# Optimization experiments

Measured on AMD Instinct MI355X. Metric: run time of the kernel, lower is better.

Reference implementation:

```python
import jax, jax.numpy as jnp
import numpy as np
from jax import lax
from jax.scipy.special import logsumexp

XY, Z, V, WS = 16, 8, 10000, 2
S = XY * XY * Z            # 2048 states
EMB, TOK, HID = 256, 100, 256
B, T, L = 8, 16, 12
EPS = 1e-5


def residual(x, w1, b1, w2, b2, g, beta):
    # ResidualLayer: relu(lin1) -> relu(lin2) -> LayerNorm(x2 + x1)
    x1 = jax.nn.relu(x @ w1.T + b1)
    x2 = jax.nn.relu(x1 @ w2.T + b2)
    h = x2 + x1
    mu = h.mean(-1, keepdims=True)
    var = ((h - mu) ** 2).mean(-1, keepdims=True)
    return (h - mu) * lax.rsqrt(var + EPS) * g + beta


def win_logmean(m, axis, ws):
    win = 2 * ws + 1
    pads = [(0, 0)] * m.ndim
    pads[axis] = (ws, ws)
    p = jnp.pad(m, pads, mode='edge')
    d = m.shape[axis]
    acc = lax.dynamic_slice_in_dim(p, 0, d, axis)
    for k in range(1, win):
        acc = jnp.logaddexp(acc, lax.dynamic_slice_in_dim(p, k, d, axis))
    return acc - jnp.log(jnp.float32(win))


def setup_inputs() -> dict:
    key = jax.random.key(0)
    it = iter(jax.random.split(key, 64))

    def rn(shape, scale=0.05):
        return jax.random.normal(next(it), shape, jnp.float32) * scale

    inp = {}
    inp['state_emb'] = jax.random.normal(next(it), (S, EMB), jnp.float32)
    inp['tok_emb'] = jax.random.normal(next(it), (V, TOK), jnp.float32)

    def res(pfx, din, dout):
        inp[pfx + '_w1'] = rn((dout, din))
        inp[pfx + '_b1'] = jnp.zeros((dout,), jnp.float32)
        inp[pfx + '_w2'] = rn((dout, dout))
        inp[pfx + '_b2'] = jnp.zeros((dout,), jnp.float32)
        inp[pfx + '_g'] = jnp.ones((dout,), jnp.float32)
        inp[pfx + '_beta'] = jnp.zeros((dout,), jnp.float32)

    res('start', EMB, HID)
    inp['start_wo'] = rn((1, HID))
    inp['start_bo'] = jnp.zeros((1,), jnp.float32)
    res('tin', EMB, HID)
    res('tout', EMB, HID)
    res('emit', EMB, TOK)
    inp['stories'] = jax.random.randint(next(it), (B, T, L), 0, V + 1)  # id V = pad
    inp['story_length'] = T
    return inp


def reference(state_emb, tok_emb,
              start_w1, start_b1, start_w2, start_b2, start_g, start_beta, start_wo, start_bo,
              tin_w1, tin_b1, tin_w2, tin_b2, tin_g, tin_beta,
              tout_w1, tout_b1, tout_w2, tout_b2, tout_g, tout_beta,
              emit_w1, emit_b1, emit_w2, emit_b2, emit_g, emit_beta,
              stories, story_length):
    # prior_log_p: [S]
    h0 = residual(state_emb, start_w1, start_b1, start_w2, start_b2, start_g, start_beta)
    priors = jax.nn.log_softmax((h0 @ start_wo.T + start_bo)[:, 0], axis=-1)

    # transition_log_p: sparse-neighbor masked [S,S] log-softmax
    h_in = residual(state_emb, tin_w1, tin_b1, tin_w2, tin_b2, tin_g, tin_beta)
    h_out = residual(state_emb, tout_w1, tout_b1, tout_w2, tout_b2, tout_g, tout_beta)
    trans = h_in @ h_out.T
    idx = jnp.arange(S)
    offs = jnp.array([0, 1, -1, XY, -XY, XY * XY, 2 * XY * XY])
    neigh = idx[:, None] + offs[None, :]                        # [S,7]
    allowed = (neigh[:, :, None] == idx[None, None, :]).any(1)  # allowed[j,i]
    trans = jax.nn.log_softmax(jnp.where(allowed, trans, -jnp.inf), axis=-1)

    # emission matrix with windowed log-mean pooling over x,y
    h_emit = residual(state_emb, emit_w1, emit_b1, emit_w2, emit_b2, emit_g, emit_beta)
    em = jax.nn.log_softmax(h_emit @ tok_emb.T, axis=1)         # [S,V]
    em = em.reshape(Z, XY, XY, V)
    em = win_logmean(em, 2, WS)   # dim -2
    em = win_logmean(em, 1, WS)   # dim -3
    em = em.reshape(S, V)
    em_pad = jnp.concatenate([em, jnp.zeros((S, 1), em.dtype)], axis=1)  # pad token
    emis = em_pad.T[stories].sum(2)                             # [B,T,S]

    # HMM forward recursion in log domain
    score0 = emis[:, 0] + priors[None, :]

    def step(score, em_t):
        new = em_t + logsumexp(trans[None, :, :] + score[:, None, :], axis=-1)
        return new, new

    _, rest = lax.scan(step, score0, jnp.moveaxis(emis[:, 1:story_length], 1, 0))
    return jnp.concatenate([score0[None], rest], axis=0)        # [T,B,S]
```

## Files before the change

### kernel.cpp

```cpp
#include <hip/hip_runtime.h>
#include <hip/hip_bf16.h>
#include <math.h>


typedef __bf16 bf16_t;
typedef __bf16 bf16x8 __attribute__((ext_vector_type(8)));
typedef float  floatx4 __attribute__((ext_vector_type(4)));
typedef short  short8  __attribute__((ext_vector_type(8)));

#define S_TOT 2048
#define NT_LSE 157
#define LSE_LD 160


struct CJob { const float* src; void* dst; int srows, scols, drows, dcols, tobf; };
struct CJobs { CJob j[12]; };

__global__ void conv_k(CJobs jobs) {
    CJob job = jobs.j[blockIdx.y];
    int total = job.drows * job.dcols;
    for (int idx = blockIdx.x * 256 + threadIdx.x; idx < total; idx += gridDim.x * 256) {
        int r = idx / job.dcols;
        int c = idx - r * job.dcols;
        float v = (r < job.srows && c < job.scols) ? job.src[(size_t)r * job.scols + c] : 0.f;
        if (job.tobf) ((bf16_t*)job.dst)[idx] = (bf16_t)v;
        else          ((float*)job.dst)[idx]  = v;
    }
}

__global__ void gather_k(const float* __restrict__ tok_emb, const int* __restrict__ stories,
                         bf16_t* __restrict__ dst) {
    int j = blockIdx.x;
    int c = threadIdx.x;
    int tok = stories[j];
    float v = (tok < 10000 && c < 100) ? tok_emb[(size_t)tok * 100 + c] : 0.f;
    dst[(size_t)j * 128 + c] = (bf16_t)v;
}

struct GJob {
    const bf16_t* A; int lda;
    const bf16_t* Bt; int ldb;
    int N, K;
    float* C; int ldc;
    const float* bias;
    const float* addm; int ldadd;
    bf16_t* Cbf; int ldcb;
    float* Pmax; float* Psum;
};
struct GJobs { GJob j[4]; };

#define BM 64
#define BN 64
#define LDT 72

template<int EPI>
__global__ __launch_bounds__(256) void gemm_k(GJobs jobs) {
    GJob jb = jobs.j[blockIdx.z];
    const int m0 = blockIdx.x * BM;
    const int n0 = blockIdx.y * BN;
    if (n0 >= jb.N) return;

    __shared__ alignas(16) bf16_t As[BM * LDT];
    __shared__ alignas(16) bf16_t Bs[BN * LDT];
    const int tid  = threadIdx.x;
    const int lane = tid & 63, wave = tid >> 6;
    const int wm = (wave & 1) * 32, wn = (wave >> 1) * 32;
    const int sr = tid >> 2, scc = (tid & 3) * 16;
    const int qm = lane & 15, qk = (lane >> 4) * 8;

    floatx4 acc[2][2];
    floatx4 zf = {0.f, 0.f, 0.f, 0.f};
#pragma unroll
    for (int i = 0; i < 2; i++)
#pragma unroll
        for (int j = 0; j < 2; j++) acc[i][j] = zf;

    for (int k0 = 0; k0 < jb.K; k0 += 64) {
        const bf16_t* Ar = jb.A + (size_t)(m0 + sr) * jb.lda + k0 + scc;
        const bf16_t* Br = jb.Bt + (size_t)(n0 + sr) * jb.ldb + k0 + scc;
        *(short8*)&As[sr * LDT + scc]     = *(const short8*)&Ar[0];
        *(short8*)&As[sr * LDT + scc + 8] = *(const short8*)&Ar[8];
        *(short8*)&Bs[sr * LDT + scc]     = *(const short8*)&Br[0];
        *(short8*)&Bs[sr * LDT + scc + 8] = *(const short8*)&Br[8];
        __syncthreads();
#pragma unroll
        for (int kk = 0; kk < 2; kk++) {
            int qo = kk * 32 + qk;
            bf16x8 a[2], b[2];
            a[0] = *(const bf16x8*)&As[(wm + qm) * LDT + qo];
            a[1] = *(const bf16x8*)&As[(wm + 16 + qm) * LDT + qo];
            b[0] = *(const bf16x8*)&Bs[(wn + qm) * LDT + qo];
            b[1] = *(const bf16x8*)&Bs[(wn + 16 + qm) * LDT + qo];
#pragma unroll
            for (int mi = 0; mi < 2; mi++)
#pragma unroll
                for (int ni = 0; ni < 2; ni++)
                    acc[mi][ni] = __builtin_amdgcn_mfma_f32_16x16x32_bf16(a[mi], b[ni], acc[mi][ni], 0, 0, 0);
        }
        __syncthreads();
    }

    const int cl = lane & 15, rq = (lane >> 4) * 4;

    if constexpr (EPI == 3) {
        __shared__ float Cs[BM][BN + 1];
#pragma unroll
        for (int mi = 0; mi < 2; mi++)
#pragma unroll
            for (int ni = 0; ni < 2; ni++)
#pragma unroll
                for (int r = 0; r < 4; r++) {
                    int lm = wm + mi * 16 + rq + r;
                    int ln2 = wn + ni * 16 + cl;
                    Cs[lm][ln2] = (n0 + ln2 < jb.N) ? acc[mi][ni][r] : -INFINITY;
                }
        __syncthreads();
        int trow = tid >> 2, part = tid & 3;
        float m = -INFINITY;
#pragma unroll
        for (int c = 0; c < 16; c++) m = fmaxf(m, Cs[trow][part * 16 + c]);
        m = fmaxf(m, __shfl_xor(m, 1));
        m = fmaxf(m, __shfl_xor(m, 2));
        float ss = 0.f;
#pragma unroll
        for (int c = 0; c < 16; c++) ss += __expf(Cs[trow][part * 16 + c] - m);
        ss += __shfl_xor(ss, 1);
        ss += __shfl_xor(ss, 2);
        if (part == 0) {
            jb.Pmax[(size_t)(m0 + trow) * LSE_LD + blockIdx.y] = m;
            jb.Psum[(size_t)(m0 + trow) * LSE_LD + blockIdx.y] = ss;
        }
    } else {
#pragma unroll
        for (int mi = 0; mi < 2; mi++)
#pragma unroll
            for (int ni = 0; ni < 2; ni++)
#pragma unroll
                for (int r = 0; r < 4; r++) {
                    int gm = m0 + wm + mi * 16 + rq + r;
                    int gn = n0 + wn + ni * 16 + cl;
                    if (gn < jb.N) {
                        float v = acc[mi][ni][r];
                        if constexpr (EPI == 0) {
                            jb.C[(size_t)gm * jb.ldc + gn] = v;
                        } else if constexpr (EPI == 1) {
                            v = fmaxf(v + jb.bias[gn], 0.f);
                            jb.C[(size_t)gm * jb.ldc + gn] = v;
                            jb.Cbf[(size_t)gm * jb.ldcb + gn] = (bf16_t)v;
                        } else {
                            v = fmaxf(v + jb.bias[gn], 0.f) + jb.addm[(size_t)gm * jb.ldadd + gn];
                            jb.C[(size_t)gm * jb.ldc + gn] = v;
                        }
                    }
                }
    }
}

struct LJob {
    const float* h; int ld, dout;
    const float* g; const float* beta;
    float* of32; int ldo;
    bf16_t* obf; int ldob; int padN;
    const float* wo; const float* bo; float* praw;
};
struct LJobs { LJob j[4]; };

__global__ __launch_bounds__(256) void ln_k(LJobs jobs) {
    LJob jb = jobs.j[blockIdx.y];
    __shared__ float red[256];
    int row = blockIdx.x, t = threadIdx.x;
    float hv = (t < jb.dout) ? jb.h[(size_t)row * jb.ld + t] : 0.f;
    red[t] = hv;
    __syncthreads();
#pragma unroll
    for (int s = 128; s > 0; s >>= 1) { if (t < s) red[t] += red[t + s]; __syncthreads(); }
    float mu = red[0] / jb.dout;
    __syncthreads();
    float d = (t < jb.dout) ? (hv - mu) : 0.f;
    red[t] = d * d;
    __syncthreads();
#pragma unroll
    for (int s = 128; s > 0; s >>= 1) { if (t < s) red[t] += red[t + s]; __syncthreads(); }
    float var = red[0] / jb.dout;
    float rstd = rsqrtf(var + 1e-5f);
    float y = 0.f;
    if (t < jb.dout) {
        y = d * rstd * jb.g[t] + jb.beta[t];
        if (jb.of32) jb.of32[(size_t)row * jb.ldo + t] = y;
        if (jb.obf)  jb.obf[(size_t)row * jb.ldob + t] = (bf16_t)y;
    } else if (jb.obf && t < jb.padN) {
        jb.obf[(size_t)row * jb.ldob + t] = (bf16_t)0.f;
    }
    if (jb.wo) {
        __syncthreads();
        red[t] = (t < jb.dout) ? y * jb.wo[t] : 0.f;
        __syncthreads();
#pragma unroll
        for (int s = 128; s > 0; s >>= 1) { if (t < s) red[t] += red[t + s]; __syncthreads(); }
        if (t == 0) jb.praw[row] = red[0] + jb.bo[0];
    }
}

__global__ __launch_bounds__(256) void trans_k(const float* __restrict__ hin,
                                               const float* __restrict__ hout,
                                               float* __restrict__ tr,
                                               const float* __restrict__ praw,
                                               float* __restrict__ plse)
{
    __shared__ float red[256];
    if (blockIdx.x == 512) {
        int t = threadIdx.x;
        float v[8];
        float m = -INFINITY;
#pragma unroll
        for (int i = 0; i < 8; i++) { v[i] = praw[t * 8 + i]; m = fmaxf(m, v[i]); }
        red[t] = m;
        __syncthreads();
#pragma unroll
        for (int s = 128; s > 0; s >>= 1) { if (t < s) red[t] = fmaxf(red[t], red[t + s]); __syncthreads(); }
        float M = red[0];
        __syncthreads();
        float ss = 0.f;
#pragma unroll
        for (int i = 0; i < 8; i++) ss += __expf(v[i] - M);
        red[t] = ss;
        __syncthreads();
#pragma unroll
        for (int s = 128; s > 0; s >>= 1) { if (t < s) red[t] += red[t + s]; __syncthreads(); }
        if (t == 0) plse[0] = M + __logf(red[0]);
        return;
    }
    const int OFFS[7] = {0, 1, -1, 16, -16, 256, 512};
    int j = blockIdx.x * 4 + (threadIdx.x >> 6);
    int lane = threadIdx.x & 63;
    float4 a = ((const float4*)(hin + (size_t)j * 256))[lane];
    float d[7];
#pragma unroll
    for (int k = 0; k < 7; k++) {
        int i = j + OFFS[k];
        float pdot = 0.f;
        if ((unsigned)i < 2048u) {
            float4 b = ((const float4*)(hout + (size_t)i * 256))[lane];
            pdot = a.x * b.x + a.y * b.y + a.z * b.z + a.w * b.w;
        }
#pragma unroll
        for (int o = 32; o > 0; o >>= 1) pdot += __shfl_down(pdot, o);
        d[k] = pdot;
    }
    if (lane == 0) {
        float m = -INFINITY;
#pragma unroll
        for (int k = 0; k < 7; k++) { int i = j + OFFS[k]; if ((unsigned)i < 2048u) m = fmaxf(m, d[k]); }
        float ss = 0.f;
#pragma unroll
        for (int k = 0; k < 7; k++) { int i = j + OFFS[k]; if ((unsigned)i < 2048u) ss += __expf(d[k] - m); }
        float l = __logf(ss);
#pragma unroll
        for (int k = 0; k < 7; k++) {
            int i = j + OFFS[k];
            tr[(size_t)j * 8 + k] = ((unsigned)i < 2048u) ? (d[k] - m - l) : -INFINITY;
        }
        tr[(size_t)j * 8 + 7] = -INFINITY;
    }
}

__global__ __launch_bounds__(256) void lse_fin_k(const float* __restrict__ Pmax,
                                                 const float* __restrict__ Psum,
                                                 float* __restrict__ lse)
{
    int s = (blockIdx.x * 256 + threadIdx.x) >> 6;
    int lane = threadIdx.x & 63;
    const float* pm = Pmax + (size_t)s * LSE_LD;
    const float* ps = Psum + (size_t)s * LSE_LD;
    float pv[3], sv[3];
    float m = -INFINITY;
#pragma unroll
    for (int i = 0; i < 3; i++) {
        int nb = i * 64 + lane;
        bool ok = nb < NT_LSE;
        pv[i] = ok ? pm[nb] : -INFINITY;
        sv[i] = ok ? ps[nb] : 0.f;
        m = fmaxf(m, pv[i]);
    }
#pragma unroll
    for (int o = 1; o < 64; o <<= 1) m = fmaxf(m, __shfl_xor(m, o));
    float ss = 0.f;
#pragma unroll
    for (int i = 0; i < 3; i++) ss += sv[i] * __expf(pv[i] - m);
#pragma unroll
    for (int o = 1; o < 64; o <<= 1) ss += __shfl_xor(ss, o);
    if (lane == 0) lse[s] = m + __logf(ss);
}

__global__ __launch_bounds__(256) void poolemis_k(const float* __restrict__ em,
                                                  const float* __restrict__ lse,
                                                  const int* __restrict__ stories,
                                                  float* __restrict__ emis)
{
    __shared__ float sm[256];
    __shared__ float sm2[256];
    int bt = blockIdx.x, z = blockIdx.y, t = threadIdx.x;
    int a = t >> 4, b = t & 15;
    float lsev = lse[z * 256 + t];
    const int* st = stories + bt * 12;
    float acc = 0.f;
    for (int l = 0; l < 12; l++) {
        int tok = st[l];
        size_t base = (size_t)(bt * 12 + l) * S_TOT + (size_t)z * 256;
        float v = em[base + t] - lsev;
        sm[t] = v;
        __syncthreads();
        float m = -INFINITY;
#pragma unroll
        for (int d = -2; d <= 2; d++) {
            int bb = b + d; bb = bb < 0 ? 0 : (bb > 15 ? 15 : bb);
            m = fmaxf(m, sm[a * 16 + bb]);
        }
        float ss = 0.f;
#pragma unroll
        for (int d = -2; d <= 2; d++) {
            int bb = b + d; bb = bb < 0 ? 0 : (bb > 15 ? 15 : bb);
            ss += __expf(sm[a * 16 + bb] - m);
        }
        sm2[t] = m + __logf(ss);
        __syncthreads();
        float m2 = -INFINITY;
#pragma unroll
        for (int d = -2; d <= 2; d++) {
            int aa = a + d; aa = aa < 0 ? 0 : (aa > 15 ? 15 : aa);
            m2 = fmaxf(m2, sm2[aa * 16 + b]);
        }
        float s2 = 0.f;
#pragma unroll
        for (int d = -2; d <= 2; d++) {
            int aa = a + d; aa = aa < 0 ? 0 : (aa > 15 ? 15 : aa);
            s2 += __expf(sm2[aa * 16 + b] - m2);
        }
        if (tok < 10000) acc += m2 + __logf(s2) - 3.2188758248682006f;
        __syncthreads();
    }
    emis[(size_t)bt * S_TOT + (size_t)z * 256 + t] = acc;
}

__global__ __launch_bounds__(1024) void fwd_k(const float* __restrict__ emm,
                                              const float* __restrict__ praw,
                                              const float* __restrict__ plse,
                                              const float* __restrict__ tr,
                                              float* __restrict__ out)
{
    const int OFFS[7] = {0, 1, -1, 16, -16, 256, 512};
    __shared__ float sc[2][S_TOT];
    int b = blockIdx.x, t = threadIdx.x;
    float pl = plse[0];
    const float* eb = emm + (size_t)b * 16 * S_TOT;

    float e[2][16];
#pragma unroll
    for (int i = 0; i < 2; i++) {
        int j = i * 1024 + t;
#pragma unroll
        for (int tt = 0; tt < 16; tt++) e[i][tt] = eb[tt * S_TOT + j];
    }
    float trj[2][7];
#pragma unroll
    for (int i = 0; i < 2; i++) {
        int j = i * 1024 + t;
        float4 lo = ((const float4*)(tr + (size_t)j * 8))[0];
        float4 hi = ((const float4*)(tr + (size_t)j * 8))[1];
        trj[i][0] = lo.x; trj[i][1] = lo.y; trj[i][2] = lo.z; trj[i][3] = lo.w;
        trj[i][4] = hi.x; trj[i][5] = hi.y; trj[i][6] = hi.z;
    }
#pragma unroll
    for (int i = 0; i < 2; i++) {
        int j = i * 1024 + t;
        float v = e[i][0] + praw[j] - pl;
        sc[0][j] = v;
        out[(size_t)b * S_TOT + j] = v;
    }
    __syncthreads();
#pragma unroll
    for (int tt = 1; tt < 16; tt++) {
        int cur = tt & 1, prv = cur ^ 1;
#pragma unroll
        for (int i = 0; i < 2; i++) {
            int j = i * 1024 + t;
            float x[7];
            float m = -INFINITY;
#pragma unroll
            for (int k = 0; k < 7; k++) {
                int ii = j + OFFS[k];
                ii = ii < 0 ? 0 : (ii > 2047 ? 2047 : ii);
                x[k] = trj[i][k] + sc[prv][ii];
                m = fmaxf(m, x[k]);
            }
            float ss = 0.f;
#pragma unroll
            for (int k = 0; k < 7; k++) ss += __expf(x[k] - m);
            float v = e[i][tt] + m + __logf(ss);
            sc[cur][j] = v;
            out[(size_t)tt * (8 * S_TOT) + (size_t)b * S_TOT + j] = v;
        }
        __syncthreads();
    }
}

extern "C" void kernel_launch(void* const* d_in, const int* in_sizes, int n_in,
                              void* d_out, int out_size, void* d_ws, size_t ws_size,
                              hipStream_t stream)
{
    (void)in_sizes; (void)n_in; (void)out_size; (void)ws_size;
    const float* state_emb  = (const float*)d_in[0];
    const float* tok_emb    = (const float*)d_in[1];
    const float* start_w1   = (const float*)d_in[2];
    const float* start_b1   = (const float*)d_in[3];
    const float* start_w2   = (const float*)d_in[4];
    const float* start_b2   = (const float*)d_in[5];
    const float* start_g    = (const float*)d_in[6];
    const float* start_beta = (const float*)d_in[7];
    const float* start_wo   = (const float*)d_in[8];
    const float* start_bo   = (const float*)d_in[9];
    const float* tin_w1     = (const float*)d_in[10];
    const float* tin_b1     = (const float*)d_in[11];
    const float* tin_w2     = (const float*)d_in[12];
    const float* tin_b2     = (const float*)d_in[13];
    const float* tin_g      = (const float*)d_in[14];
    const float* tin_beta   = (const float*)d_in[15];
    const float* tout_w1    = (const float*)d_in[16];
    const float* tout_b1    = (const float*)d_in[17];
    const float* tout_w2    = (const float*)d_in[18];
    const float* tout_b2    = (const float*)d_in[19];
    const float* tout_g     = (const float*)d_in[20];
    const float* tout_beta  = (const float*)d_in[21];
    const float* emit_w1    = (const float*)d_in[22];
    const float* emit_b1    = (const float*)d_in[23];
    const float* emit_w2    = (const float*)d_in[24];
    const float* emit_b2    = (const float*)d_in[25];
    const float* emit_g     = (const float*)d_in[26];
    const float* emit_beta  = (const float*)d_in[27];
    const int*   stories    = (const int*)d_in[28];
    float* out = (float*)d_out;

    char* base = (char*)d_ws;
    size_t off = 0;
    auto carve = [&](size_t bytes) -> char* {
        char* r = base + off;
        off = (off + bytes + 255) & ~(size_t)255;
        return r;
    };

    bf16_t* se_bf   = (bf16_t*)carve((size_t)2048 * 256 * 2);
    bf16_t* tok_bf  = (bf16_t*)carve((size_t)10048 * 128 * 2);
    bf16_t* w_s1    = (bf16_t*)carve((size_t)256 * 256 * 2);
    bf16_t* w_s2    = (bf16_t*)carve((size_t)256 * 256 * 2);
    bf16_t* w_i1    = (bf16_t*)carve((size_t)256 * 256 * 2);
    bf16_t* w_i2    = (bf16_t*)carve((size_t)256 * 256 * 2);
    bf16_t* w_o1    = (bf16_t*)carve((size_t)256 * 256 * 2);
    bf16_t* w_o2    = (bf16_t*)carve((size_t)256 * 256 * 2);
    bf16_t* w_e1    = (bf16_t*)carve((size_t)128 * 256 * 2);
    bf16_t* w_e2    = (bf16_t*)carve((size_t)128 * 128 * 2);
    float*  eb1     = (float*)carve(128 * 4);
    float*  eb2     = (float*)carve(128 * 4);
    bf16_t* hemit   = (bf16_t*)carve((size_t)2048 * 128 * 2);
    float*  hin     = (float*)carve((size_t)2048 * 256 * 4);
    float*  hout    = (float*)carve((size_t)2048 * 256 * 4);
    float*  praw    = (float*)carve((size_t)2048 * 4);
    float*  plse    = (float*)carve(256);
    float*  trans   = (float*)carve((size_t)2048 * 8 * 4);
    bf16_t* tokused = (bf16_t*)carve((size_t)1536 * 128 * 2);
    float*  pmax    = (float*)carve((size_t)2048 * LSE_LD * 4);
    float*  psum    = (float*)carve((size_t)2048 * LSE_LD * 4);
    float*  lse     = (float*)carve((size_t)2048 * 4);

    size_t ovl = off;
    auto carveA = [&](size_t bytes) -> char* {
        char* r = base + ovl;
        ovl = (ovl + bytes + 255) & ~(size_t)255;
        return r;
    };
    float*  x1f_s  = (float*)carveA((size_t)2048 * 256 * 4);
    float*  x1f_i  = (float*)carveA((size_t)2048 * 256 * 4);
    float*  x1f_o  = (float*)carveA((size_t)2048 * 256 * 4);
    float*  x1f_e  = (float*)carveA((size_t)2048 * 128 * 4);
    bf16_t* x1b_s  = (bf16_t*)carveA((size_t)2048 * 256 * 2);
    bf16_t* x1b_i  = (bf16_t*)carveA((size_t)2048 * 256 * 2);
    bf16_t* x1b_o  = (bf16_t*)carveA((size_t)2048 * 256 * 2);
    bf16_t* x1b_e  = (bf16_t*)carveA((size_t)2048 * 128 * 2);
    float*  htmp_s = (float*)carveA((size_t)2048 * 256 * 4);
    float*  htmp_i = (float*)carveA((size_t)2048 * 256 * 4);
    float*  htmp_o = (float*)carveA((size_t)2048 * 256 * 4);
    float*  htmp_e = (float*)carveA((size_t)2048 * 128 * 4);

    size_t ovlB = off;
    auto carveB = [&](size_t bytes) -> char* {
        char* r = base + ovlB;
        ovlB = (ovlB + bytes + 255) & ~(size_t)255;
        return r;
    };
    float* em   = (float*)carveB((size_t)1536 * 2048 * 4);
    float* emis = (float*)carveB((size_t)128 * 2048 * 4);

    CJobs cj;
    cj.j[0]  = {state_emb, se_bf, 2048, 256, 2048, 256, 1};
    cj.j[1]  = {tok_emb,   tok_bf, 10000, 100, 10048, 128, 1};
    cj.j[2]  = {start_w1,  w_s1, 256, 256, 256, 256, 1};
    cj.j[3]  = {start_w2,  w_s2, 256, 256, 256, 256, 1};
    cj.j[4]  = {tin_w1,    w_i1, 256, 256, 256, 256, 1};
    cj.j[5]  = {tin_w2,    w_i2, 256, 256, 256, 256, 1};
    cj.j[6]  = {tout_w1,   w_o1, 256, 256, 256, 256, 1};
    cj.j[7]  = {tout_w2,   w_o2, 256, 256, 256, 256, 1};
    cj.j[8]  = {emit_w1,   w_e1, 100, 256, 128, 256, 1};
    cj.j[9]  = {emit_w2,   w_e2, 100, 100, 128, 128, 1};
    cj.j[10] = {emit_b1,   eb1, 1, 100, 1, 128, 0};
    cj.j[11] = {emit_b2,   eb2, 1, 100, 1, 128, 0};
    conv_k<<<dim3(160, 12), 256, 0, stream>>>(cj);
    gather_k<<<1536, 128, 0, stream>>>(tok_emb, stories, tokused);

    GJobs g1;
    g1.j[0] = {se_bf, 256, w_s1, 256, 256, 256, x1f_s, 256, start_b1, nullptr, 0, x1b_s, 256, nullptr, nullptr};
    g1.j[1] = {se_bf, 256, w_i1, 256, 256, 256, x1f_i, 256, tin_b1,   nullptr, 0, x1b_i, 256, nullptr, nullptr};
    g1.j[2] = {se_bf, 256, w_o1, 256, 256, 256, x1f_o, 256, tout_b1,  nullptr, 0, x1b_o, 256, nullptr, nullptr};
    g1.j[3] = {se_bf, 256, w_e1, 256, 128, 256, x1f_e, 128, eb1,      nullptr, 0, x1b_e, 128, nullptr, nullptr};
    gemm_k<1><<<dim3(32, 4, 4), 256, 0, stream>>>(g1);

    GJobs g2;
    g2.j[0] = {x1b_s, 256, w_s2, 256, 256, 256, htmp_s, 256, start_b2, x1f_s, 256, nullptr, 0, nullptr, nullptr};
    g2.j[1] = {x1b_i, 256, w_i2, 256, 256, 256, htmp_i, 256, tin_b2,   x1f_i, 256, nullptr, 0, nullptr, nullptr};
    g2.j[2] = {x1b_o, 256, w_o2, 256, 256, 256, htmp_o, 256, tout_b2,  x1f_o, 256, nullptr, 0, nullptr, nullptr};
    g2.j[3] = {x1b_e, 128, w_e2, 128, 128, 128, htmp_e, 128, eb2,      x1f_e, 128, nullptr, 0, nullptr, nullptr};
    gemm_k<2><<<dim3(32, 4, 4), 256, 0, stream>>>(g2);

    LJobs lj;
    lj.j[0] = {htmp_s, 256, 256, start_g, start_beta, nullptr, 0, nullptr, 0, 0, start_wo, start_bo, praw};
    lj.j[1] = {htmp_i, 256, 256, tin_g,   tin_beta,   hin, 256, nullptr, 0, 0, nullptr, nullptr, nullptr};
    lj.j[2] = {htmp_o, 256, 256, tout_g,  tout_beta,  hout, 256, nullptr, 0, 0, nullptr, nullptr, nullptr};
    lj.j[3] = {htmp_e, 128, 100, emit_g,  emit_beta,  nullptr, 0, hemit, 128, 128, nullptr, nullptr, nullptr};
    ln_k<<<dim3(2048, 4), 256, 0, stream>>>(lj);

    trans_k<<<513, 256, 0, stream>>>(hin, hout, trans, praw, plse);

    GJobs g3;
    g3.j[0] = {hemit, 128, tok_bf, 128, 10000, 128, nullptr, 0, nullptr, nullptr, 0, nullptr, 0, pmax, psum};
    gemm_k<3><<<dim3(32, NT_LSE, 1), 256, 0, stream>>>(g3);
    lse_fin_k<<<512, 256, 0, stream>>>(pmax, psum, lse);

    GJobs g0;
    g0.j[0] = {tokused, 128, hemit, 128, 2048, 128, em, 2048, nullptr, nullptr, 0, nullptr, 0, nullptr, nullptr};
    gemm_k<0><<<dim3(24, 32, 1), 256, 0, stream>>>(g0);
    poolemis_k<<<dim3(128, 8), 256, 0, stream>>>(em, lse, stories, emis);

    fwd_k<<<8, 1024, 0, stream>>>(emis, praw, plse, trans, out);
}
```

Baseline: 222.4 us.

## Fuse token gather, emission GEMM and window pooling into one kernel

Measured after the change: 221.8 us. Within noise of the previous version (-0.3%).

```diff
diff --git a/kernel.cpp b/kernel.cpp
--- a/kernel.cpp
+++ b/kernel.cpp
@@ -26,15 +26,6 @@
         if (job.tobf) ((bf16_t*)job.dst)[idx] = (bf16_t)v;
         else          ((float*)job.dst)[idx]  = v;
     }
-}
-
-__global__ void gather_k(const float* __restrict__ tok_emb, const int* __restrict__ stories,
-                         bf16_t* __restrict__ dst) {
-    int j = blockIdx.x;
-    int c = threadIdx.x;
-    int tok = stories[j];
-    float v = (tok < 10000 && c < 100) ? tok_emb[(size_t)tok * 100 + c] : 0.f;
-    dst[(size_t)j * 128 + c] = (bf16_t)v;
 }
 
 struct GJob {
@@ -292,35 +283,76 @@
     if (lane == 0) lse[s] = m + __logf(ss);
 }
 
-__global__ __launch_bounds__(256) void poolemis_k(const float* __restrict__ em,
-                                                  const float* __restrict__ lse,
-                                                  const int* __restrict__ stories,
-                                                  float* __restrict__ emis)
+#define ELDT 136
+__global__ __launch_bounds__(256) void empool_k(
+    const float* __restrict__ tok_emb, const int* __restrict__ stories,
+    const bf16_t* __restrict__ hemit, const float* __restrict__ lse,
+    float* __restrict__ emis)
 {
-    __shared__ float sm[256];
+    __shared__ alignas(16) bf16_t As[16 * ELDT];
+    __shared__ float Cs[16][260];
     __shared__ float sm2[256];
-    int bt = blockIdx.x, z = blockIdx.y, t = threadIdx.x;
-    int a = t >> 4, b = t & 15;
-    float lsev = lse[z * 256 + t];
-    const int* st = stories + bt * 12;
-    float acc = 0.f;
+    __shared__ int stok[12];
+    const int bt = blockIdx.x, z = blockIdx.y, t = threadIdx.x;
+    if (t < 12) stok[t] = stories[bt * 12 + t];
+    __syncthreads();
+    {
+        int row = t >> 4, c0 = (t & 15) * 8;
+        int tok = (row < 12) ? stok[row] : 10000;
+        const float* src = tok_emb + (size_t)tok * 100;
+#pragma unroll
+        for (int c = 0; c < 8; c++) {
+            int cc = c0 + c;
+            float v = (tok < 10000 && cc < 100) ? src[cc] : 0.f;
+            As[row * ELDT + cc] = (bf16_t)v;
+        }
+    }
+    __syncthreads();
+
+    const int lane = t & 63, wave = t >> 6;
+    const int qm = lane & 15, q = lane >> 4;
+    floatx4 acc[4];
+    floatx4 zf = {0.f, 0.f, 0.f, 0.f};
+#pragma unroll
+    for (int j = 0; j < 4; j++) acc[j] = zf;
+
+#pragma unroll
+    for (int kk = 0; kk < 4; kk++) {
+        bf16x8 a = *(const bf16x8*)&As[qm * ELDT + kk * 32 + q * 8];
+#pragma unroll
+        for (int j = 0; j < 4; j++) {
+            int nrow = z * 256 + (wave * 4 + j) * 16 + qm;
+            bf16x8 b = *(const bf16x8*)&hemit[(size_t)nrow * 128 + kk * 32 + q * 8];
+            acc[j] = __builtin_amdgcn_mfma_f32_16x16x32_bf16(a, b, acc[j], 0, 0, 0);
+        }
+    }
+    {
+        const int cl = lane & 15, rq = (lane >> 4) * 4;
+#pragma unroll
+        for (int j = 0; j < 4; j++) {
+            int n = (wave * 4 + j) * 16 + cl;
+            float ls = lse[z * 256 + n];
+#pragma unroll
+            for (int r = 0; r < 4; r++)
+                Cs[rq + r][n] = acc[j][r] - ls;
+        }
+    }
+    __syncthreads();
+
+    const int a = t >> 4, b = t & 15;
+    float accum = 0.f;
     for (int l = 0; l < 12; l++) {
-        int tok = st[l];
-        size_t base = (size_t)(bt * 12 + l) * S_TOT + (size_t)z * 256;
-        float v = em[base + t] - lsev;
-        sm[t] = v;
-        __syncthreads();
         float m = -INFINITY;
 #pragma unroll
         for (int d = -2; d <= 2; d++) {
             int bb = b + d; bb = bb < 0 ? 0 : (bb > 15 ? 15 : bb);
-            m = fmaxf(m, sm[a * 16 + bb]);
+            m = fmaxf(m, Cs[l][a * 16 + bb]);
         }
         float ss = 0.f;
 #pragma unroll
         for (int d = -2; d <= 2; d++) {
             int bb = b + d; bb = bb < 0 ? 0 : (bb > 15 ? 15 : bb);
-            ss += __expf(sm[a * 16 + bb] - m);
+            ss += __expf(Cs[l][a * 16 + bb] - m);
         }
         sm2[t] = m + __logf(ss);
         __syncthreads();
@@ -336,10 +368,10 @@
             int aa = a + d; aa = aa < 0 ? 0 : (aa > 15 ? 15 : aa);
             s2 += __expf(sm2[aa * 16 + b] - m2);
         }
-        if (tok < 10000) acc += m2 + __logf(s2) - 3.2188758248682006f;
-        __syncthreads();
-    }
-    emis[(size_t)bt * S_TOT + (size_t)z * 256 + t] = acc;
+        if (stok[l] < 10000) accum += m2 + __logf(s2) - 3.2188758248682006f;
+        __syncthreads();
+    }
+    emis[(size_t)bt * S_TOT + (size_t)z * 256 + t] = accum;
 }
 
 __global__ __launch_bounds__(1024) void fwd_k(const float* __restrict__ emm,
@@ -466,10 +498,10 @@
     float*  praw    = (float*)carve((size_t)2048 * 4);
     float*  plse    = (float*)carve(256);
     float*  trans   = (float*)carve((size_t)2048 * 8 * 4);
-    bf16_t* tokused = (bf16_t*)carve((size_t)1536 * 128 * 2);
     float*  pmax    = (float*)carve((size_t)2048 * LSE_LD * 4);
     float*  psum    = (float*)carve((size_t)2048 * LSE_LD * 4);
     float*  lse     = (float*)carve((size_t)2048 * 4);
+    float*  emis    = (float*)carve((size_t)128 * 2048 * 4);
 
     size_t ovl = off;
     auto carveA = [&](size_t bytes) -> char* {
@@ -490,15 +522,6 @@
     float*  htmp_o = (float*)carveA((size_t)2048 * 256 * 4);
     float*  htmp_e = (float*)carveA((size_t)2048 * 128 * 4);
 
-    size_t ovlB = off;
-    auto carveB = [&](size_t bytes) -> char* {
-        char* r = base + ovlB;
-        ovlB = (ovlB + bytes + 255) & ~(size_t)255;
-        return r;
-    };
-    float* em   = (float*)carveB((size_t)1536 * 2048 * 4);
-    float* emis = (float*)carveB((size_t)128 * 2048 * 4);
-
     CJobs cj;
     cj.j[0]  = {state_emb, se_bf, 2048, 256, 2048, 256, 1};
     cj.j[1]  = {tok_emb,   tok_bf, 10000, 100, 10048, 128, 1};
@@ -513,7 +536,6 @@
     cj.j[10] = {emit_b1,   eb1, 1, 100, 1, 128, 0};
     cj.j[11] = {emit_b2,   eb2, 1, 100, 1, 128, 0};
     conv_k<<<dim3(160, 12), 256, 0, stream>>>(cj);
-    gather_k<<<1536, 128, 0, stream>>>(tok_emb, stories, tokused);
 
     GJobs g1;
     g1.j[0] = {se_bf, 256, w_s1, 256, 256, 256, x1f_s, 256, start_b1, nullptr, 0, x1b_s, 256, nullptr, nullptr};
@@ -543,10 +565,7 @@
     gemm_k<3><<<dim3(32, NT_LSE, 1), 256, 0, stream>>>(g3);
     lse_fin_k<<<512, 256, 0, stream>>>(pmax, psum, lse);
 
-    GJobs g0;
-    g0.j[0] = {tokused, 128, hemit, 128, 2048, 128, em, 2048, nullptr, nullptr, 0, nullptr, 0, nullptr, nullptr};
-    gemm_k<0><<<dim3(24, 32, 1), 256, 0, stream>>>(g0);
-    poolemis_k<<<dim3(128, 8), 256, 0, stream>>>(em, lse, stories, emis);
+    empool_k<<<dim3(128, 8), 256, 0, stream>>>(tok_emb, stories, hemit, lse, emis);
 
     fwd_k<<<8, 1024, 0, stream>>>(emis, praw, plse, trans, out);
 }
```
